# Kernel optimization log

Hardware: AMD Instinct MI355X
Metric: run time of the kernel (lower is better)

The kernel has to match this reference:

```python
import jax, jax.numpy as jnp
import numpy as np

NOISE_STD = 0.005
ALPHA = 0.2


def setup_inputs() -> dict:
    key = jax.random.key(0)
    k = jax.random.split(key, 6)
    B, S, I, H, O = 64, 512, 128, 2048, 128
    x = jax.random.normal(k[0], (B, S, I), jnp.float32)
    noise = jax.random.normal(k[1], (B, S, H), jnp.float32)
    wi = jax.random.normal(k[2], (I, H), jnp.float32) / np.float32(np.sqrt(I))
    wrec = jax.random.normal(k[3], (H, H), jnp.float32) / np.float32(np.sqrt(H))
    wout = jax.random.normal(k[4], (H, O), jnp.float32) / np.float32(np.sqrt(H))
    g = 0.9 * jnp.ones((H, 1), jnp.float32)
    h0 = jax.random.normal(k[5], (H,), jnp.float32)
    return {"x": x, "noise": noise, "wi": wi, "wrec": wrec, "wout": wout, "g": g, "h0": h0}


def reference(x, noise, wi, wrec, wout, g, h0):
    # linear=True => non_linearity is identity (torch.clone)
    B, S, _ = x.shape
    H = h0.shape[0]
    gT = g[:, 0]                      # [H]
    wrecT = wrec.T                    # [H, H]

    r0 = h0                           # identity nonlinearity
    out0 = jnp.broadcast_to(r0 @ wout, (B, wout.shape[1]))  # output[:, 0, :]
    h_init = jnp.broadcast_to(h0, (B, H))

    def step(h, inp):
        xi, ni = inp                  # [B, I], [B, H]
        r = h                         # identity nonlinearity of previous h
        h_new = h + NOISE_STD * ni + ALPHA * (-h + (gT * r) @ wrecT + xi @ wi)
        r_new = h_new
        return h_new, r_new @ wout    # output at step i+1

    # steps i = 0 .. S-2 use input[:, i] and noise[:, i]
    xs = (jnp.swapaxes(x[:, :-1], 0, 1), jnp.swapaxes(noise[:, :-1], 0, 1))
    _, outs = jax.lax.scan(step, h_init, xs)   # [S-1, B, O]

    output = jnp.concatenate([out0[:, None, :], jnp.swapaxes(outs, 0, 1)], axis=1)
    return output  # [B, S, O]
```

## Files before the change

kernel.cpp:

```cpp
#include <hip/hip_runtime.h>

typedef _Float16 half8 __attribute__((ext_vector_type(8)));
typedef float float4v __attribute__((ext_vector_type(4)));
typedef unsigned short ushort8 __attribute__((ext_vector_type(8)));

#define ALD(p)     __hip_atomic_load((p), __ATOMIC_RELAXED, __HIP_MEMORY_SCOPE_AGENT)
#define AST(p, v)  __hip_atomic_store((p), (v), __ATOMIC_RELAXED, __HIP_MEMORY_SCOPE_AGENT)

__device__ __forceinline__ float bf2f(unsigned short u) {
    union { unsigned int i; float f; } v; v.i = ((unsigned int)u) << 16; return v.f;
}
__device__ __forceinline__ unsigned short f2bf(float f) {
    union { float f; unsigned int i; } v; v.f = f;
    unsigned int r = (v.i + 0x7FFFu + ((v.i >> 16) & 1u)) >> 16;
    return (unsigned short)r;
}
__device__ __forceinline__ float ld_in(const void* p, size_t i, int bf) {
    return bf ? bf2f(((const unsigned short*)p)[i]) : ((const float*)p)[i];
}
__device__ __forceinline__ int detect_bf16(const void* g) {
    return *(const unsigned int*)g == 0x3F663F66u;
}
__device__ __forceinline__ int cperm(int q) {
    return (q & ~31) + ((q & 1) << 4) + ((q & 31) >> 1);
}
__device__ __forceinline__ int chunk_bad(unsigned long long a, unsigned long long b) {
    return ((unsigned int)a == 0xFFFFFFFFu) | ((unsigned int)(a >> 32) == 0xFFFFFFFFu) |
           ((unsigned int)b == 0xFFFFFFFFu) | ((unsigned int)(b >> 32) == 0xFFFFFFFFu);
}

__global__ __launch_bounds__(256) void prep_kernel(
    const void* __restrict__ wout, const void* __restrict__ g,
    const void* __restrict__ wrec, const void* __restrict__ wi,
    const void* __restrict__ h0,
    _Float16* __restrict__ woutB, half8* __restrict__ WgB,
    _Float16* __restrict__ Hist0)
{
    const int bf = detect_bf16(g);
    size_t idx = (size_t)blockIdx.x * 256 + threadIdx.x;
    if (idx < 262144) {
        int q = (int)(idx >> 7), o = (int)(idx & 127);
        int c = cperm(q);
        woutB[(((size_t)(q >> 3)) * 128 + o) * 8 + (q & 7)] =
            (_Float16)ld_in(wout, (size_t)c * 128 + o, bf);
    } else if (idx < 819200) {
        size_t i2 = idx - 262144;
        int kc = (int)(i2 >> 11), n = (int)(i2 & 2047);
        half8 v;
        if (kc < 256) {
#pragma unroll
            for (int j = 0; j < 8; ++j) {
                int c = cperm(kc * 8 + j);
                v[j] = (_Float16)(0.2f * ld_in(g, c, bf) *
                                  ld_in(wrec, (size_t)n * 2048 + c, bf));
            }
        } else {
#pragma unroll
            for (int j = 0; j < 8; ++j) {
                int i = (kc - 256) * 8 + j;
                v[j] = (_Float16)(0.2f * ld_in(wi, (size_t)i * 2048 + n, bf));
            }
        }
        WgB[(size_t)kc * 2048 + n] = v;
    } else {
        size_t i3 = idx - 819200;
        int kc = (int)(i3 >> 9);
        int j  = (int)(i3 & 7);
        Hist0[i3] = (_Float16)ld_in(h0, cperm(kc * 8 + j), bf);
    }
}

__global__ __launch_bounds__(256, 1) void rnn_persist(
    const void* __restrict__ x, const void* __restrict__ noise,
    const void* __restrict__ g, const void* __restrict__ h0,
    const half8* __restrict__ WgB, _Float16* __restrict__ Hist)
{
    __shared__ __align__(16) char lds_pool[147456];
    float4v* red = (float4v*)lds_pool;

    const int bf   = detect_bf16(g);
    const int tid  = threadIdx.x;
    const int lane = tid & 63;
    const int w    = tid >> 6;
    const int l15  = lane & 15;
    const int quad = lane >> 4;
    const int grp    = blockIdx.x >> 6;
    const int nb     = blockIdx.x & 63;
    const int n_base = nb * 32;
    const int b_base = grp * 16;
    const int pbase  = w * 17;
    const int HC     = (w == 3) ? 13 : 17;

    half8 Wb0[17], Wb1[17];
#pragma unroll
    for (int kk = 0; kk < 17; ++kk) {
        int kc = (pbase + kk) * 4 + quad;
        Wb0[kk] = WgB[(size_t)kc * 2048 + n_base + l15];
        Wb1[kk] = WgB[(size_t)kc * 2048 + n_base + 16 + l15];
    }

    float4v h[2];
    if (w == 0) {
#pragma unroll
        for (int nt = 0; nt < 2; ++nt) {
            float hv = ld_in(h0, n_base + nt * 16 + l15, bf);
            h[nt][0] = hv; h[nt][1] = hv; h[nt][2] = hv; h[nt][3] = hv;
        }
    }

    const int voff = quad * 1024 + (b_base + l15) * 16;
    const int poff = 3072 + b_base * 16 + 252;

    unsigned int D = 120;

    for (int t = 0; t < 511; ++t) {
        unsigned long long anchor = __builtin_amdgcn_s_memrealtime();

        float nz[2][4];
        if (w == 0) {
#pragma unroll
            for (int nt = 0; nt < 2; ++nt)
#pragma unroll
                for (int r = 0; r < 4; ++r)
                    nz[nt][r] = ld_in(noise,
                        ((size_t)(b_base + quad * 4 + r) * 512 + t) * 2048 +
                        n_base + nt * 16 + l15, bf);
        }
        half8 xa[4];
        if (w == 3) {
#pragma unroll
            for (int c = 0; c < 4; ++c) {
                size_t xoff = ((size_t)(b_base + l15) * 512 + t) * 128 + c * 32 + quad * 8;
                if (bf) {
                    ushort8 xv = *(const ushort8*)((const unsigned short*)x + xoff);
#pragma unroll
                    for (int j = 0; j < 8; ++j) xa[c][j] = (_Float16)bf2f(xv[j]);
                } else {
                    const float* xp = (const float*)x + xoff;
                    float4v x0 = *(const float4v*)xp;
                    float4v x1 = *(const float4v*)(xp + 4);
#pragma unroll
                    for (int j = 0; j < 4; ++j) { xa[c][j] = (_Float16)x0[j]; xa[c][j+4] = (_Float16)x1[j]; }
                }
            }
        }

        const char* At = (const char*)Hist + (size_t)t * 262144;

        if (t) {
            while ((unsigned int)(__builtin_amdgcn_s_memrealtime() - anchor) < D) { }
        }

        unsigned long long a0[17], a1[17];
#pragma unroll
        for (int kk = 0; kk < 17; ++kk) {
            if (kk < HC) {
                const unsigned long long* p = (const unsigned long long*)
                    (At + ((size_t)(pbase + kk) << 12) + voff);
                a0[kk] = ALD(p);
                a1[kk] = ALD(p + 1);
            }
        }
        unsigned int inv = 0;
#pragma unroll
        for (int kk = 0; kk < 17; ++kk) {
            if (kk < HC) {
                if (chunk_bad(a0[kk], a1[kk])) inv |= 1u << kk;
            }
        }
        const int miss = (__ballot(inv != 0) != 0ull);
        if (miss) {
            int kprobe = pbase + ((lane < HC) ? lane : 0);
            const unsigned int* pp = (const unsigned int*)
                (At + ((size_t)kprobe << 12) + poff);
            for (;;) {
                unsigned int pv = ALD(pp);
                if (__ballot(pv != 0xFFFFFFFFu) == ~0ull) break;
                __builtin_amdgcn_s_sleep(1);
            }
            asm volatile("" ::: "memory");
            while (__ballot(inv != 0)) {
#pragma unroll
                for (int kk = 0; kk < 17; ++kk) {
                    if (kk < HC) {
                        if (inv & (1u << kk)) {
                            const unsigned long long* p = (const unsigned long long*)
                                (At + ((size_t)(pbase + kk) << 12) + voff);
                            a0[kk] = ALD(p);
                            a1[kk] = ALD(p + 1);
                            if (!chunk_bad(a0[kk], a1[kk])) inv &= ~(1u << kk);
                        }
                    }
                }
            }
        }
        if (t) {
            if (miss) D = (D + 24 > 320u) ? 320u : D + 24;
            else      D = (D >= 2u) ? D - 2 : 0u;
        }

        float4v acc[2] = {{0.f,0.f,0.f,0.f},{0.f,0.f,0.f,0.f}};
        if (w < 3) {
#pragma unroll
            for (int kk = 0; kk < 17; ++kk) {
                union { unsigned long long u[2]; half8 v; } au;
                au.u[0] = a0[kk]; au.u[1] = a1[kk];
                acc[0] = __builtin_amdgcn_mfma_f32_16x16x32_f16(au.v, Wb0[kk], acc[0], 0, 0, 0);
                acc[1] = __builtin_amdgcn_mfma_f32_16x16x32_f16(au.v, Wb1[kk], acc[1], 0, 0, 0);
            }
        } else {
#pragma unroll
            for (int kk = 0; kk < 13; ++kk) {
                union { unsigned long long u[2]; half8 v; } au;
                au.u[0] = a0[kk]; au.u[1] = a1[kk];
                acc[0] = __builtin_amdgcn_mfma_f32_16x16x32_f16(au.v, Wb0[kk], acc[0], 0, 0, 0);
                acc[1] = __builtin_amdgcn_mfma_f32_16x16x32_f16(au.v, Wb1[kk], acc[1], 0, 0, 0);
            }
#pragma unroll
            for (int c = 0; c < 4; ++c) {
                acc[0] = __builtin_amdgcn_mfma_f32_16x16x32_f16(xa[c], Wb0[13 + c], acc[0], 0, 0, 0);
                acc[1] = __builtin_amdgcn_mfma_f32_16x16x32_f16(xa[c], Wb1[13 + c], acc[1], 0, 0, 0);
            }
        }

        if (w) {
            int base = (((t & 1) * 3 + (w - 1)) * 64 + lane) * 2;
            red[base]     = acc[0];
            red[base + 1] = acc[1];
        }
        __syncthreads();

        if (w == 0) {
#pragma unroll
            for (int q = 0; q < 3; ++q) {
                int base = (((t & 1) * 3 + q) * 64 + lane) * 2;
                acc[0] += red[base];
                acc[1] += red[base + 1];
            }
            unsigned int* Hd = (unsigned int*)(Hist + (size_t)(t + 1) * 131072);
            const int kcl = nb * 4 + (l15 >> 2);
            unsigned int* dst0 = Hd + ((size_t)kcl * 64 + b_base + quad * 4) * 4 + (l15 & 3);
#pragma unroll
            for (int r = 0; r < 4; ++r) {
                float hn0 = 0.8f * h[0][r] + 0.005f * nz[0][r] + acc[0][r];
                float hn1 = 0.8f * h[1][r] + 0.005f * nz[1][r] + acc[1][r];
                h[0][r] = hn0; h[1][r] = hn1;
                union { _Float16 hf; unsigned short s; } u0, u1;
                u0.hf = (_Float16)hn0; u1.hf = (_Float16)hn1;
                AST(dst0 + r * 4, ((unsigned int)u1.s << 16) | u0.s);
            }
        }
    }
}

__global__ __launch_bounds__(256) void out_gemm(
    const _Float16* __restrict__ Hist, const _Float16* __restrict__ woutB,
    const void* __restrict__ g, void* __restrict__ out)
{
    const int bf = detect_bf16(g);
    const int tid = threadIdx.x;
    const int lane = tid & 63;
    const int w = tid >> 6;
    const int l15 = lane & 15, quad = lane >> 4;
    const int m0 = blockIdx.x * 64 + w * 16;
    const int tt = m0 >> 6;
    const int bb = m0 & 63;

    float4v acc[8] = {};
    const _Float16* Ar = Hist + (size_t)tt * 131072 +
                         ((size_t)(bb + l15)) * 8 + (size_t)quad * 512;
#pragma unroll 4
    for (int ki = 0; ki < 64; ++ki) {
        half8 a = *(const half8*)(Ar + (size_t)ki * 2048);
#pragma unroll
        for (int nt = 0; nt < 8; ++nt) {
            half8 b = *(const half8*)(woutB + ((size_t)((ki * 4 + quad) * 128 + nt * 16 + l15)) * 8);
            acc[nt] = __builtin_amdgcn_mfma_f32_16x16x32_f16(a, b, acc[nt], 0, 0, 0);
        }
    }
#pragma unroll
    for (int nt = 0; nt < 8; ++nt) {
#pragma unroll
        for (int r = 0; r < 4; ++r) {
            int row = m0 + quad * 4 + r;
            int b = row & 63, t = row >> 6;
            int o = nt * 16 + l15;
            size_t oi = ((size_t)b * 512 + t) * 128 + o;
            if (bf) ((unsigned short*)out)[oi] = f2bf(acc[nt][r]);
            else    ((float*)out)[oi] = acc[nt][r];
        }
    }
}

extern "C" void kernel_launch(void* const* d_in, const int* in_sizes, int n_in,
                              void* d_out, int out_size, void* d_ws, size_t ws_size,
                              hipStream_t stream)
{
    const void* x     = d_in[0];
    const void* noise = d_in[1];
    const void* wi    = d_in[2];
    const void* wrec  = d_in[3];
    const void* wout  = d_in[4];
    const void* g     = d_in[5];
    const void* h0    = d_in[6];

    char* ws = (char*)d_ws;
    _Float16* woutB   = (_Float16*)(ws + 4096);
    half8*    WgB     = (half8*)(ws + 4096 + 524288);
    _Float16* Hist    = (_Float16*)(ws + 9441280);

    hipMemsetAsync((char*)Hist + 262144, 0xFF, (size_t)511 * 262144, stream);
    prep_kernel<<<3712, 256, 0, stream>>>(wout, g, wrec, wi, h0, woutB, WgB, Hist);
    rnn_persist<<<256, 256, 0, stream>>>(x, noise, g, h0, WgB, Hist);
    out_gemm<<<512, 256, 0, stream>>>(Hist, woutB, g, d_out);
}
```

Before: 2.440 ms.

## Balance K-split across waves and parallelize reduction and state update over all waves

Each of the four waves now handles 16 recurrent K-chunks plus one x-input chunk, replacing the uneven 17/17/17/13 split. All waves write partials to LDS, and each wave reduces one output row component and performs the h update, noise load and store. Before, only wave 0 did that work serially. The MFMA chain is split into two independent accumulators to shorten dependency latency, and the adaptive spin delay parameters are retuned.

```diff
diff --git a/kernel.cpp b/kernel.cpp
--- a/kernel.cpp
+++ b/kernel.cpp
@@ -27,6 +27,11 @@
 __device__ __forceinline__ int chunk_bad(unsigned long long a, unsigned long long b) {
     return ((unsigned int)a == 0xFFFFFFFFu) | ((unsigned int)(a >> 32) == 0xFFFFFFFFu) |
            ((unsigned int)b == 0xFFFFFFFFu) | ((unsigned int)(b >> 32) == 0xFFFFFFFFu);
+}
+__device__ __forceinline__ float compw(float4v v, int w) {
+    float a = (w & 1) ? v[1] : v[0];
+    float b = (w & 1) ? v[3] : v[2];
+    return (w & 2) ? b : a;
 }
 
 __global__ __launch_bounds__(256) void prep_kernel(
@@ -88,60 +93,54 @@
     const int nb     = blockIdx.x & 63;
     const int n_base = nb * 32;
     const int b_base = grp * 16;
-    const int pbase  = w * 17;
-    const int HC     = (w == 3) ? 13 : 17;
+    const int ubase  = w * 16;
 
     half8 Wb0[17], Wb1[17];
 #pragma unroll
-    for (int kk = 0; kk < 17; ++kk) {
-        int kc = (pbase + kk) * 4 + quad;
+    for (int kk = 0; kk < 16; ++kk) {
+        int kc = (ubase + kk) * 4 + quad;
         Wb0[kk] = WgB[(size_t)kc * 2048 + n_base + l15];
         Wb1[kk] = WgB[(size_t)kc * 2048 + n_base + 16 + l15];
     }
-
-    float4v h[2];
-    if (w == 0) {
-#pragma unroll
-        for (int nt = 0; nt < 2; ++nt) {
-            float hv = ld_in(h0, n_base + nt * 16 + l15, bf);
-            h[nt][0] = hv; h[nt][1] = hv; h[nt][2] = hv; h[nt][3] = hv;
-        }
-    }
+    {
+        int kcx = 256 + w * 4 + quad;
+        Wb0[16] = WgB[(size_t)kcx * 2048 + n_base + l15];
+        Wb1[16] = WgB[(size_t)kcx * 2048 + n_base + 16 + l15];
+    }
+
+    float h[2];
+#pragma unroll
+    for (int nt = 0; nt < 2; ++nt)
+        h[nt] = ld_in(h0, n_base + nt * 16 + l15, bf);
 
     const int voff = quad * 1024 + (b_base + l15) * 16;
     const int poff = 3072 + b_base * 16 + 252;
+    const int myrow = b_base + quad * 4 + w;
 
     unsigned int D = 120;
 
     for (int t = 0; t < 511; ++t) {
         unsigned long long anchor = __builtin_amdgcn_s_memrealtime();
 
-        float nz[2][4];
-        if (w == 0) {
-#pragma unroll
-            for (int nt = 0; nt < 2; ++nt)
-#pragma unroll
-                for (int r = 0; r < 4; ++r)
-                    nz[nt][r] = ld_in(noise,
-                        ((size_t)(b_base + quad * 4 + r) * 512 + t) * 2048 +
-                        n_base + nt * 16 + l15, bf);
-        }
-        half8 xa[4];
-        if (w == 3) {
-#pragma unroll
-            for (int c = 0; c < 4; ++c) {
-                size_t xoff = ((size_t)(b_base + l15) * 512 + t) * 128 + c * 32 + quad * 8;
-                if (bf) {
-                    ushort8 xv = *(const ushort8*)((const unsigned short*)x + xoff);
-#pragma unroll
-                    for (int j = 0; j < 8; ++j) xa[c][j] = (_Float16)bf2f(xv[j]);
-                } else {
-                    const float* xp = (const float*)x + xoff;
-                    float4v x0 = *(const float4v*)xp;
-                    float4v x1 = *(const float4v*)(xp + 4);
-#pragma unroll
-                    for (int j = 0; j < 4; ++j) { xa[c][j] = (_Float16)x0[j]; xa[c][j+4] = (_Float16)x1[j]; }
-                }
+        float nz[2];
+#pragma unroll
+        for (int nt = 0; nt < 2; ++nt)
+            nz[nt] = ld_in(noise,
+                ((size_t)myrow * 512 + t) * 2048 + n_base + nt * 16 + l15, bf);
+
+        half8 xa;
+        {
+            size_t xoff = ((size_t)(b_base + l15) * 512 + t) * 128 + w * 32 + quad * 8;
+            if (bf) {
+                ushort8 xv = *(const ushort8*)((const unsigned short*)x + xoff);
+#pragma unroll
+                for (int j = 0; j < 8; ++j) xa[j] = (_Float16)bf2f(xv[j]);
+            } else {
+                const float* xp = (const float*)x + xoff;
+                float4v x0 = *(const float4v*)xp;
+                float4v x1 = *(const float4v*)(xp + 4);
+#pragma unroll
+                for (int j = 0; j < 4; ++j) { xa[j] = (_Float16)x0[j]; xa[j+4] = (_Float16)x1[j]; }
             }
         }
 
@@ -151,28 +150,23 @@
             while ((unsigned int)(__builtin_amdgcn_s_memrealtime() - anchor) < D) { }
         }
 
-        unsigned long long a0[17], a1[17];
-#pragma unroll
-        for (int kk = 0; kk < 17; ++kk) {
-            if (kk < HC) {
-                const unsigned long long* p = (const unsigned long long*)
-                    (At + ((size_t)(pbase + kk) << 12) + voff);
-                a0[kk] = ALD(p);
-                a1[kk] = ALD(p + 1);
-            }
+        unsigned long long a0[16], a1[16];
+#pragma unroll
+        for (int kk = 0; kk < 16; ++kk) {
+            const unsigned long long* p = (const unsigned long long*)
+                (At + ((size_t)(ubase + kk) << 12) + voff);
+            a0[kk] = ALD(p);
+            a1[kk] = ALD(p + 1);
         }
         unsigned int inv = 0;
 #pragma unroll
-        for (int kk = 0; kk < 17; ++kk) {
-            if (kk < HC) {
-                if (chunk_bad(a0[kk], a1[kk])) inv |= 1u << kk;
-            }
-        }
+        for (int kk = 0; kk < 16; ++kk)
+            if (chunk_bad(a0[kk], a1[kk])) inv |= 1u << kk;
+
         const int miss = (__ballot(inv != 0) != 0ull);
         if (miss) {
-            int kprobe = pbase + ((lane < HC) ? lane : 0);
             const unsigned int* pp = (const unsigned int*)
-                (At + ((size_t)kprobe << 12) + poff);
+                (At + ((size_t)(ubase + (lane & 15)) << 12) + poff);
             for (;;) {
                 unsigned int pv = ALD(pp);
                 if (__ballot(pv != 0xFFFFFFFFu) == ~0ull) break;
@@ -181,74 +175,59 @@
             asm volatile("" ::: "memory");
             while (__ballot(inv != 0)) {
 #pragma unroll
-                for (int kk = 0; kk < 17; ++kk) {
-                    if (kk < HC) {
-                        if (inv & (1u << kk)) {
-                            const unsigned long long* p = (const unsigned long long*)
-                                (At + ((size_t)(pbase + kk) << 12) + voff);
-                            a0[kk] = ALD(p);
-                            a1[kk] = ALD(p + 1);
-                            if (!chunk_bad(a0[kk], a1[kk])) inv &= ~(1u << kk);
-                        }
+                for (int kk = 0; kk < 16; ++kk) {
+                    if (inv & (1u << kk)) {
+                        const unsigned long long* p = (const unsigned long long*)
+                            (At + ((size_t)(ubase + kk) << 12) + voff);
+                        a0[kk] = ALD(p);
+                        a1[kk] = ALD(p + 1);
+                        if (!chunk_bad(a0[kk], a1[kk])) inv &= ~(1u << kk);
                     }
                 }
             }
         }
         if (t) {
-            if (miss) D = (D + 24 > 320u) ? 320u : D + 24;
-            else      D = (D >= 2u) ? D - 2 : 0u;
-        }
-
-        float4v acc[2] = {{0.f,0.f,0.f,0.f},{0.f,0.f,0.f,0.f}};
-        if (w < 3) {
-#pragma unroll
-            for (int kk = 0; kk < 17; ++kk) {
-                union { unsigned long long u[2]; half8 v; } au;
-                au.u[0] = a0[kk]; au.u[1] = a1[kk];
-                acc[0] = __builtin_amdgcn_mfma_f32_16x16x32_f16(au.v, Wb0[kk], acc[0], 0, 0, 0);
-                acc[1] = __builtin_amdgcn_mfma_f32_16x16x32_f16(au.v, Wb1[kk], acc[1], 0, 0, 0);
-            }
-        } else {
-#pragma unroll
-            for (int kk = 0; kk < 13; ++kk) {
-                union { unsigned long long u[2]; half8 v; } au;
-                au.u[0] = a0[kk]; au.u[1] = a1[kk];
-                acc[0] = __builtin_amdgcn_mfma_f32_16x16x32_f16(au.v, Wb0[kk], acc[0], 0, 0, 0);
-                acc[1] = __builtin_amdgcn_mfma_f32_16x16x32_f16(au.v, Wb1[kk], acc[1], 0, 0, 0);
-            }
-#pragma unroll
-            for (int c = 0; c < 4; ++c) {
-                acc[0] = __builtin_amdgcn_mfma_f32_16x16x32_f16(xa[c], Wb0[13 + c], acc[0], 0, 0, 0);
-                acc[1] = __builtin_amdgcn_mfma_f32_16x16x32_f16(xa[c], Wb1[13 + c], acc[1], 0, 0, 0);
-            }
-        }
-
-        if (w) {
-            int base = (((t & 1) * 3 + (w - 1)) * 64 + lane) * 2;
-            red[base]     = acc[0];
-            red[base + 1] = acc[1];
+            if (miss) D = (D + 16 > 400u) ? 400u : D + 16;
+            else      D = (D >= 1u) ? D - 1 : 0u;
+        }
+
+        float4v c0[2] = {{0.f,0.f,0.f,0.f},{0.f,0.f,0.f,0.f}};
+        float4v c1[2] = {{0.f,0.f,0.f,0.f},{0.f,0.f,0.f,0.f}};
+#pragma unroll
+        for (int kk = 0; kk < 16; kk += 2) {
+            union { unsigned long long u[2]; half8 v; } ae, ao;
+            ae.u[0] = a0[kk];     ae.u[1] = a1[kk];
+            ao.u[0] = a0[kk + 1]; ao.u[1] = a1[kk + 1];
+            c0[0] = __builtin_amdgcn_mfma_f32_16x16x32_f16(ae.v, Wb0[kk],     c0[0], 0, 0, 0);
+            c0[1] = __builtin_amdgcn_mfma_f32_16x16x32_f16(ae.v, Wb1[kk],     c0[1], 0, 0, 0);
+            c1[0] = __builtin_amdgcn_mfma_f32_16x16x32_f16(ao.v, Wb0[kk + 1], c1[0], 0, 0, 0);
+            c1[1] = __builtin_amdgcn_mfma_f32_16x16x32_f16(ao.v, Wb1[kk + 1], c1[1], 0, 0, 0);
+        }
+        c0[0] = __builtin_amdgcn_mfma_f32_16x16x32_f16(xa, Wb0[16], c0[0], 0, 0, 0);
+        c0[1] = __builtin_amdgcn_mfma_f32_16x16x32_f16(xa, Wb1[16], c0[1], 0, 0, 0);
+
+        {
+            int base = (((t & 1) * 4 + w) * 64 + lane) * 2;
+            red[base]     = c0[0] + c1[0];
+            red[base + 1] = c0[1] + c1[1];
         }
         __syncthreads();
 
-        if (w == 0) {
-#pragma unroll
-            for (int q = 0; q < 3; ++q) {
-                int base = (((t & 1) * 3 + q) * 64 + lane) * 2;
-                acc[0] += red[base];
-                acc[1] += red[base + 1];
-            }
+        {
+            int pb = ((t & 1) * 4) * 64 * 2 + lane * 2;
+            float s0 = compw(red[pb],           w) + compw(red[pb + 128],     w)
+                     + compw(red[pb + 256],     w) + compw(red[pb + 384],     w);
+            float s1 = compw(red[pb + 1],       w) + compw(red[pb + 129],     w)
+                     + compw(red[pb + 257],     w) + compw(red[pb + 385],     w);
+            float hn0 = 0.8f * h[0] + 0.005f * nz[0] + s0;
+            float hn1 = 0.8f * h[1] + 0.005f * nz[1] + s1;
+            h[0] = hn0; h[1] = hn1;
+            union { _Float16 hf; unsigned short s; } u0, u1;
+            u0.hf = (_Float16)hn0; u1.hf = (_Float16)hn1;
+            unsigned int pv = ((unsigned int)u1.s << 16) | u0.s;
             unsigned int* Hd = (unsigned int*)(Hist + (size_t)(t + 1) * 131072);
             const int kcl = nb * 4 + (l15 >> 2);
-            unsigned int* dst0 = Hd + ((size_t)kcl * 64 + b_base + quad * 4) * 4 + (l15 & 3);
-#pragma unroll
-            for (int r = 0; r < 4; ++r) {
-                float hn0 = 0.8f * h[0][r] + 0.005f * nz[0][r] + acc[0][r];
-                float hn1 = 0.8f * h[1][r] + 0.005f * nz[1][r] + acc[1][r];
-                h[0][r] = hn0; h[1][r] = hn1;
-                union { _Float16 hf; unsigned short s; } u0, u1;
-                u0.hf = (_Float16)hn0; u1.hf = (_Float16)hn1;
-                AST(dst0 + r * 4, ((unsigned int)u1.s << 16) | u0.s);
-            }
+            AST(Hd + ((size_t)kcl * 64 + myrow) * 4 + (l15 & 3), pv);
         }
     }
 }
```

New measurement: 2.036 ms. 16.6% less time.
